# Kernel tuning notes

Measured on AMD Instinct MI355X. Metric: run time of the kernel, lower is better.

The kernel has to match this reference:

```python
import jax, jax.numpy as jnp
import numpy as np
from jax import lax

PS = 4  # patchsize

def conv2d(x, w, b, pad, dil=1):
    y = lax.conv_general_dilated(x, w, (1, 1), [(pad, pad), (pad, pad)],
                                 rhs_dilation=(dil, dil),
                                 dimension_numbers=('NCHW', 'OIHW', 'NCHW'))
    return y + b[None, :, None, None]

def instance_norm(x, eps=1e-5):
    mu = x.mean(axis=(2, 3), keepdims=True)
    var = x.var(axis=(2, 3), keepdims=True)
    return (x - mu) / jnp.sqrt(var + eps)

def lrelu(x):
    return jnp.where(x >= 0, x, 0.2 * x)

def setup_inputs() -> dict:
    key = jax.random.key(0)
    ks = jax.random.split(key, 20)
    B, C, H, W = 16, 256, 64, 64
    nh, nw = H // PS, W // PS
    N = nh * nw
    s = 0.05
    return {
        'x': jax.random.normal(ks[0], (B, C, H, W), jnp.float32),
        'mask': jax.random.uniform(ks[1], (B, 1, H, W), jnp.float32),
        'dis': jax.random.normal(ks[2], (N, N), jnp.float32),
        'lap_a': jnp.ones((1,), jnp.float32),
        'Wq': jax.random.normal(ks[3], (C, C, 1, 1), jnp.float32) * s,
        'bq': jax.random.normal(ks[4], (C,), jnp.float32) * s,
        'Wk': jax.random.normal(ks[5], (C, C, 1, 1), jnp.float32) * s,
        'bk': jax.random.normal(ks[6], (C,), jnp.float32) * s,
        'Wv': jax.random.normal(ks[7], (C, C, 1, 1), jnp.float32) * s,
        'bv': jax.random.normal(ks[8], (C,), jnp.float32) * s,
        'noise_q': jax.random.normal(ks[9], (B, C, nh, PS, nw, PS), jnp.float32),
        'noise_k': jax.random.normal(ks[10], (B, C, nh, PS, nw, PS), jnp.float32),
        'noise_v': jax.random.normal(ks[11], (B, C, nh, PS, nw, PS), jnp.float32),
        'W_out': jax.random.normal(ks[12], (C, C, 3, 3), jnp.float32) * s,
        'b_out': jax.random.normal(ks[13], (C,), jnp.float32) * s,
        'W1': jax.random.normal(ks[14], (C, C, 3, 3), jnp.float32) * s,
        'b1': jax.random.normal(ks[15], (C,), jnp.float32) * s,
        'W2': jax.random.normal(ks[16], (C, C, 3, 3), jnp.float32) * s,
        'b2': jax.random.normal(ks[17], (C,), jnp.float32) * s,
    }

def _patchify(t, noise, B, C, nh, nw):
    # (B,C,H,W) -> (B,C,nh,PS,nw,PS) + noise -> (B, nh*nw, C*PS*PS)
    t = t.reshape(B, C, nh, PS, nw, PS) + noise
    t = t.transpose(0, 2, 4, 1, 3, 5).reshape(B, nh * nw, C * PS * PS)
    return t

def reference(x, mask, dis, lap_a, Wq, bq, Wk, bk, Wv, bv,
              noise_q, noise_k, noise_v, W_out, b_out, W1, b1, W2, b2):
    B, C, H, W = x.shape
    nh, nw = H // PS, W // PS
    N = nh * nw
    head = PS * 4
    Cp = C * PS * PS
    d = Cp // head

    residual = x
    q = _patchify(conv2d(x, Wq, bq, 0), noise_q, B, C, nh, nw)
    k = _patchify(conv2d(x, Wk, bk, 0), noise_k, B, C, nh, nw)
    v = _patchify(conv2d(x, Wv, bv, 0), noise_v, B, C, nh, nw)

    dis_b = jax.nn.softplus(lap_a)[0] * dis  # (N, N)

    qh = q.reshape(B, N, head, d)
    kh = k.reshape(B, N, head, d)
    vh = v.reshape(B, N, head, d)

    # scores: (head, B, N, N); bias added BEFORE scaling, as in the original
    scores = jnp.einsum('bnhd,bmhd->hbnm', qh, kh)
    scores = (scores + dis_b) / jnp.sqrt(jnp.asarray(d, scores.dtype))

    # mask: patch mean < 0.5 masks key positions
    m = mask.reshape(B, 1, nh, PS, nw, PS).transpose(0, 2, 4, 1, 3, 5)
    m = m.reshape(B, N, PS * PS).mean(-1) < 0.5  # (B, N) bool
    m = jnp.broadcast_to(m[:, None, :], (B, N, N))  # (B, N, N)
    scores = jnp.where(m[None], -jnp.inf, scores)

    p = jax.nn.softmax(scores, axis=-1)
    out = jnp.einsum('hbnm,bmhd->bnhd', p, vh).reshape(B, N, Cp)

    # un-patchify: (B,N,Cp) -> (B,nh,nw,C,PS,PS) -> (B,C,H,W)
    out = out.reshape(B, nh, nw, C, PS, PS).transpose(0, 3, 1, 4, 2, 5).reshape(B, C, H, W)
    out = lrelu(conv2d(out, W_out, b_out, 1)) + residual

    # feed-forward: conv(dil=2) -> IN -> lrelu -> conv -> IN -> lrelu, residual
    y = lrelu(instance_norm(conv2d(out, W1, b1, 2, dil=2)))
    y = lrelu(instance_norm(conv2d(y, W2, b2, 1)))
    return out + y
```

## Files before the change

### kernel.cpp

```cpp
#include <hip/hip_runtime.h>
#include <cstdint>
#include <cstddef>

typedef _Float16 f16;
typedef _Float16 f16x8 __attribute__((ext_vector_type(8)));
typedef _Float16 f16x4 __attribute__((ext_vector_type(4)));
typedef float    f32x4 __attribute__((ext_vector_type(4)));

#define MFMA16(a,b,c) __builtin_amdgcn_mfma_f32_16x16x32_f16((a),(b),(c),0,0,0)

__device__ __forceinline__ float lrelu(float v){ return v >= 0.f ? v : 0.2f*v; }

__device__ __forceinline__ void async_copy16(const f16* g, f16* l){
  __builtin_amdgcn_global_load_lds(
      (const __attribute__((address_space(1))) void*)(uintptr_t)(const void*)g,
      (__attribute__((address_space(3))) void*)(uint32_t)(uintptr_t)(void*)l,
      16, 0, 0);
}


__global__ __launch_bounds__(256) void k_prep1x1(
    const float* __restrict__ wq, const float* __restrict__ wk, const float* __restrict__ wv,
    f16* __restrict__ oq, f16* __restrict__ ok, f16* __restrict__ ov)
{
  int i = blockIdx.x*256 + threadIdx.x;
  int sel = i >> 16, r = i & 65535;
  const float* s = sel==0 ? wq : (sel==1 ? wk : wv);
  f16* d = sel==0 ? oq : (sel==1 ? ok : ov);
  d[r] = (f16)s[r];
}

__global__ __launch_bounds__(256) void k_prep3x3(
    const float* __restrict__ w0, const float* __restrict__ w1, const float* __restrict__ w2,
    f16* __restrict__ o0, f16* __restrict__ o1, f16* __restrict__ o2)
{
  int i = blockIdx.x*256 + threadIdx.x;
  int sel = i / 589824;
  int r = i - sel*589824;
  int t = r >> 16; int rr = r & 65535; int co = rr >> 8; int ci = rr & 255;
  const float* s = sel==0 ? w0 : (sel==1 ? w1 : w2);
  f16* d = sel==0 ? o0 : (sel==1 ? o1 : o2);
  d[r] = (f16)s[(co*256 + ci)*9 + t];
}

__global__ __launch_bounds__(256) void k_pmask(const float* __restrict__ mask, float* __restrict__ pm)
{
  int t = blockIdx.x*256 + threadIdx.x;
  int b = t >> 8, n = t & 255;
  int y0 = (n>>4)<<2, x0 = (n&15)<<2;
  const float* mb = mask + b*4096;
  float s = 0.f;
  #pragma unroll
  for (int i=0;i<4;++i)
    #pragma unroll
    for (int j=0;j<4;++j) s += mb[(y0+i)*64 + x0+j];
  pm[t] = (s*(1.f/16.f) < 0.5f) ? 1.f : 0.f;
}

__global__ __launch_bounds__(256) void k_nchw2nhwc(
    const float* __restrict__ src, const float2* __restrict__ st, f16* __restrict__ dst)
{
  int idx = blockIdx.x;
  int y = idx & 63, b = idx >> 6;
  int tid = threadIdx.x;
  __shared__ f16 T[64*264];

  {
    const float* row = src + (size_t)(b*256+tid)*4096 + y*64;
    float mu = 0.f, ri = 1.f;
    bool doin = (st != nullptr);
    if (doin){ float2 s = st[b*256+tid]; mu = s.x; ri = s.y; }
    #pragma unroll
    for (int j=0;j<16;++j){
      float4 u = *(const float4*)(row + j*4);
      int x = j*4;
      float a0=(u.x-mu)*ri, a1=(u.y-mu)*ri, a2=(u.z-mu)*ri, a3=(u.w-mu)*ri;
      if (doin){ a0=lrelu(a0); a1=lrelu(a1); a2=lrelu(a2); a3=lrelu(a3); }
      T[(x+0)*264+tid]=(f16)a0; T[(x+1)*264+tid]=(f16)a1;
      T[(x+2)*264+tid]=(f16)a2; T[(x+3)*264+tid]=(f16)a3;
    }
  }
  __syncthreads();
  {
    int oct = tid & 31, pxl = tid >> 5;
    #pragma unroll
    for (int p=0;p<8;++p){
      int px = p*8 + pxl;
      *(uint4*)&dst[((size_t)((b*64+y)*64+px)<<8) + oct*8] = *(const uint4*)&T[px*264 + oct*8];
    }
  }
}

__global__ __launch_bounds__(256, 4) void k_qkv(
    const f16* __restrict__ xh,
    const f16* __restrict__ wq, const f16* __restrict__ wk, const f16* __restrict__ wv,
    const float* __restrict__ bq, const float* __restrict__ bk, const float* __restrict__ bv,
    const float* __restrict__ nq, const float* __restrict__ nk, const float* __restrict__ nv,
    f16* __restrict__ Qp, f16* __restrict__ Kp, f16* __restrict__ Vt)
{
  int idx = blockIdx.x;
  int yt  = idx & 15; idx >>= 4;
  int cot = idx & 3;  idx >>= 2;
  int b   = idx & 15; idx >>= 4;
  int sel = idx;
  int tid = threadIdx.x;
  int wave = tid>>6, lane = tid&63, quad = lane>>4, l16 = lane&15;
  int co0 = cot*64, y0 = yt*4;

  const f16*  W    = sel==0 ? wq : (sel==1 ? wk : wv);
  const float* bias= sel==0 ? bq : (sel==1 ? bk : bv);
  const float* nz  = sel==0 ? nq : (sel==1 ? nk : nv);

  __shared__ f16 smem[20480];

  f32x4 acc[16];
  #pragma unroll
  for (int i=0;i<16;++i){ acc[i][0]=0.f; acc[i][1]=0.f; acc[i][2]=0.f; acc[i][3]=0.f; }

  int g8 = (((lane&3) ^ ((lane>>3)&3)) << 3);
  const f16* Wrow = W + ((co0 + wave*16 + (lane>>2))<<8) + g8;
  const f16* Xrow = xh + (((size_t)((b*64 + y0)*64))<<8) + g8;

  auto stage = [&](int buf, int kc){
    int ci0 = kc<<5;
    f16* Ab = smem + buf*2048;
    f16* Bb = smem + 4096 + buf*8192;
    async_copy16(Wrow + ci0, Ab + wave*512);
    #pragma unroll
    for (int j=0;j<4;++j){
      int px = j*64 + wave*16 + (lane>>2);
      async_copy16(Xrow + ((size_t)px<<8) + ci0, Bb + (j*64 + wave*16)*32);
    }
  };

  stage(0, 0);
  #pragma unroll
  for (int kc=0; kc<8; ++kc){
    int cur = kc & 1;
    if (kc < 7){
      stage(cur^1, kc+1);
      asm volatile("s_waitcnt vmcnt(5)\n\ts_barrier" ::: "memory");
    } else {
      asm volatile("s_waitcnt vmcnt(0)\n\ts_barrier" ::: "memory");
    }
    const f16* Al = smem + cur*2048;
    const f16* Bl = smem + 4096 + cur*8192;
    f16x8 af = *(const f16x8*)&Al[(wave*16+l16)*32 + ((quad ^ ((l16>>1)&3))<<3)];
    #pragma unroll
    for (int nt=0;nt<16;++nt){
      int bidx = (nt>>2)*64 + (nt&3)*16 + l16;
      f16x8 bf = *(const f16x8*)&Bl[bidx*32 + ((quad ^ ((bidx>>1)&3))<<3)];
      acc[nt] = MFMA16(af, bf, acc[nt]);
    }
    asm volatile("s_waitcnt lgkmcnt(0)\n\ts_barrier" ::: "memory");
  }

  int cob = co0 + wave*16 + quad*4;
  int h0 = cot*4, pr = yt;
  float bs[4];
  #pragma unroll
  for (int r=0;r<4;++r) bs[r] = bias[cob+r];

  const float* nzb = nz + ((size_t)(b*256 + co0) << 12) + y0*64;

  #pragma unroll
  for (int half=0; half<2; ++half){
    #pragma unroll
    for (int p=0;p<8;++p){
      int i = p*256 + tid;
      int c32 = i>>6, px0 = (i&63)*4;
      float4 u = *(const float4*)(nzb + (((size_t)(half*32 + c32))<<12) + px0);
      f16x4 h4; h4[0]=(f16)u.x; h4[1]=(f16)u.y; h4[2]=(f16)u.z; h4[3]=(f16)u.w;
      *(f16x4*)&smem[c32*256 + (px0 ^ (((c32>>2)&3)<<4))] = h4;
    }
    __syncthreads();
    if ((wave>>1) == half){
      #pragma unroll
      for (int nt=0;nt<16;++nt){
        int px = (nt>>2)*64 + (nt&3)*16 + l16;
        int n_ = (nt&3)*4 + (l16>>2);
        int ddb = (quad<<6) + ((nt>>2)<<2) + (l16&3);
        #pragma unroll
        for (int r=0;r<4;++r){
          int c32 = ((wave&1)<<4) + (quad<<2) + r;
          float nzv = (float)smem[c32*256 + (px ^ (((c32>>2)&3)<<4))];
          float v = acc[nt][r] + bs[r] + nzv;
          int dd = ddb + (r<<4);
          if (sel < 2){
            int row = ((wave&1)<<4) + n_;
            smem[8192 + row*280 + dd + ((dd>>6)<<3)] = (f16)v;
          } else {
            smem[8192 + ((wave&1)*4128) + dd*16 + ((dd>>6)<<3) + n_] = (f16)v;
          }
        }
      }
    }
    __syncthreads();
    if (sel < 2){
      f16* dst = sel==0 ? Qp : Kp;
      #pragma unroll
      for (int pass=0; pass<4; ++pass){
        int rowi = pass*8 + (tid>>5);
        int ch  = tid & 31;
        uint4 v = *(const uint4*)&smem[8192 + rowi*280 + ch*8 + ((ch>>3)<<3)];
        int grow = half*32 + rowi;
        *(uint4*)&dst[((b*16 + h0 + (grow>>4))<<16) + ((pr*16 + (grow&15))<<8) + ch*8] = v;
      }
    } else {
      #pragma unroll
      for (int p=0;p<4;++p){
        int i = p*256 + tid;
        int rw = i>>1, hf = i&1;
        int dd = rw & 255;
        uint4 v = *(const uint4*)&smem[8192 + (rw>>8)*4128 + dd*16 + ((dd>>6)<<3) + hf*8];
        *(uint4*)&Vt[((b*16 + h0 + half*2 + (rw>>8))<<16) + (dd<<8) + pr*16 + hf*8] = v;
      }
    }
    __syncthreads();
  }
}

__global__ __launch_bounds__(256) void k_attn(
    const f16* __restrict__ Qp, const f16* __restrict__ Kp, const f16* __restrict__ Vt,
    const float* __restrict__ dis, const float* __restrict__ lap_a,
    const float* __restrict__ pm, f16* __restrict__ attn)
{
  int idx = blockIdx.x;
  int nt = idx & 3; idx >>= 2;
  int h  = idx & 15; idx >>= 4;
  int b  = idx;
  int tid = threadIdx.x, wave = tid>>6, lane = tid&63, quad = lane>>4, l16 = lane&15;
  int n0 = nt*64;
  int bh = (b*16 + h) << 16;

  __shared__ f16 smem[25344];
  f16* Ql  = smem;
  f16* KVl = smem + 16896;

  {
    int row = tid>>2, part = (tid&3)*64;
    const uint4* s = (const uint4*)&Qp[bh + ((n0+row)<<8) + part];
    uint4* d = (uint4*)&Ql[row*264 + part];
    #pragma unroll
    for (int j=0;j<8;++j) d[j] = s[j];
  }

  float splus = log1pf(expf(lap_a[0]));

  f32x4 sacc[16];
  #pragma unroll
  for (int i=0;i<16;++i){ sacc[i][0]=0.f; sacc[i][1]=0.f; sacc[i][2]=0.f; sacc[i][3]=0.f; }

  #pragma unroll
  for (int mc=0; mc<8; ++mc){
    __syncthreads();
    {
      int row = tid>>3, part = (tid&7)*32;
      const uint4* s = (const uint4*)&Kp[bh + ((mc*32+row)<<8) + part];
      uint4* d = (uint4*)&KVl[row*264 + part];
      #pragma unroll
      for (int j=0;j<4;++j) d[j] = s[j];
    }
    __syncthreads();
    #pragma unroll
    for (int kk=0;kk<8;++kk){
      f16x8 af = *(const f16x8*)&Ql[(wave*16+l16)*264 + kk*32 + quad*8];
      #pragma unroll
      for (int j=0;j<2;++j){
        f16x8 bf = *(const f16x8*)&KVl[(j*16+l16)*264 + kk*32 + quad*8];
        sacc[mc*2+j] = MFMA16(af, bf, sacc[mc*2+j]);
      }
    }
  }

  int nrow_base = wave*16 + quad*4;
  float pmv[16];
  #pragma unroll
  for (int t=0;t<16;++t) pmv[t] = pm[b*256 + t*16 + l16];

  #pragma unroll
  for (int r=0;r<4;++r){
    int n = n0 + nrow_base + r;
    float sv[16];
    float mx = -1e30f;
    #pragma unroll
    for (int t=0;t<16;++t){
      float s = sacc[t][r];
      s = (s + splus * dis[n*256 + t*16 + l16]) * 0.0625f;
      s = (pmv[t] > 0.5f) ? -1e30f : s;
      sv[t] = s;
      mx = fmaxf(mx, s);
    }
    #pragma unroll
    for (int off=1; off<16; off<<=1) mx = fmaxf(mx, __shfl_xor(mx, off, 64));
    float sum = 0.f;
    #pragma unroll
    for (int t=0;t<16;++t){ float e = __expf(sv[t]-mx); sv[t]=e; sum += e; }
    #pragma unroll
    for (int off=1; off<16; off<<=1) sum += __shfl_xor(sum, off, 64);
    float inv = 1.f/sum;
    #pragma unroll
    for (int t=0;t<16;++t) Ql[(nrow_base + r)*264 + t*16 + l16] = (f16)(sv[t]*inv);
  }

  f32x4 oacc[16];
  #pragma unroll
  for (int i=0;i<16;++i){ oacc[i][0]=0.f; oacc[i][1]=0.f; oacc[i][2]=0.f; oacc[i][3]=0.f; }

  for (int dc=0; dc<8; ++dc){
    __syncthreads();
    {
      int row = tid>>3, part = (tid&7)*32;
      const uint4* s = (const uint4*)&Vt[bh + ((dc*32+row)<<8) + part];
      uint4* d = (uint4*)&KVl[row*264 + part];
      #pragma unroll
      for (int j=0;j<4;++j) d[j] = s[j];
    }
    __syncthreads();
    #pragma unroll
    for (int kk=0;kk<8;++kk){
      f16x8 af = *(const f16x8*)&Ql[(wave*16+l16)*264 + kk*32 + quad*8];
      #pragma unroll
      for (int j=0;j<2;++j){
        f16x8 bf = *(const f16x8*)&KVl[(j*16+l16)*264 + kk*32 + quad*8];
        oacc[dc*2+j] = MFMA16(af, bf, oacc[dc*2+j]);
      }
    }
  }

  __syncthreads();
  #pragma unroll
  for (int dc=0; dc<8; ++dc){
    #pragma unroll
    for (int j=0;j<2;++j){
      int dd = dc*32 + j*16 + l16;
      int c_ = dd>>4;
      int pi = (dd>>2)&3, pj = dd&3;
      #pragma unroll
      for (int r=0;r<4;++r){
        int nl = nrow_base + r;
        int y_ = ((nl>>4)<<2) + pi;
        int x  = ((nl&15)<<2) + pj;
        smem[(y_*64 + x)*24 + c_] = (f16)oacc[dc*2+j][r];
      }
    }
  }
  __syncthreads();
  #pragma unroll
  for (int p=0;p<4;++p){
    int pix = p*256 + tid;
    int y_ = pix>>6, x = pix&63;
    uint4 v0 = *(const uint4*)&smem[pix*24];
    uint4 v1 = *(const uint4*)&smem[pix*24 + 8];
    size_t o = ((size_t)((b*64 + nt*16 + y_)*64 + x)<<8) + h*16;
    *(uint4*)&attn[o]     = v0;
    *(uint4*)&attn[o + 8] = v1;
  }
}

template<int DIL, int MODE>
__global__ __launch_bounds__(256) void k_conv3(
    const f16* __restrict__ in, const f16* __restrict__ Wt, const float* __restrict__ bias,
    const float* __restrict__ resid, float* __restrict__ outf, f16* __restrict__ outh)
{
  int idx = blockIdx.x;
  int yt  = idx & 15; idx >>= 4;
  int cot = idx & 3;  idx >>= 2;
  int b   = idx;
  int y0 = yt*4, co0 = cot*64;
  int tid = threadIdx.x;
  int wave = tid>>6, lane = tid&63, quad = lane>>4, l16 = lane&15;

  __shared__ float cs4[8192];
  f16* Al = (f16*)cs4;
  f16* Bl = (f16*)cs4 + 7680;

  f32x4 acc[16];
  #pragma unroll
  for (int i=0;i<16;++i){ acc[i][0]=0.f; acc[i][1]=0.f; acc[i][2]=0.f; acc[i][3]=0.f; }

  constexpr int PXR = 64 + 2*DIL;
  constexpr int NU4 = 16*PXR;

  for (int ky=0; ky<3; ++ky){
    int yb = y0 + DIL*(ky-1);
    for (int kc=0; kc<8; ++kc){
      int ci0 = kc*32;
      {
        int aco = tid>>2, ap = (tid&3)*8;
        #pragma unroll
        for (int kx=0;kx<3;++kx)
          *(uint4*)&Al[kx*2560 + aco*40 + ap] =
              *(const uint4*)&Wt[((ky*3+kx)<<16) + ((co0+aco)<<8) + ci0 + ap];
      }
      #pragma unroll
      for (int p=0;p<5;++p){
        int i = p*256 + tid;
        if (i < NU4){
          int px = i>>2, oct = i&3;
          int yr = px / PXR, xp = px - yr*PXR;
          int yy = yb + yr, xx = xp - DIL;
          uint4 v = make_uint4(0u,0u,0u,0u);
          if (yy>=0 && yy<64 && xx>=0 && xx<64)
            v = *(const uint4*)&in[((size_t)((b*64+yy)*64+xx)<<8) + ci0 + oct*8];
          int si = yr*68 + xp;
          *(uint4*)&Bl[si*32 + ((oct ^ ((si>>1)&3))<<3)] = v;
        }
      }
      __syncthreads();
      #pragma unroll
      for (int kx=0;kx<3;++kx){
        f16x8 af = *(const f16x8*)&Al[kx*2560 + (wave*16+l16)*40 + quad*8];
        #pragma unroll
        for (int nt=0;nt<16;++nt){
          int bidx = (nt>>2)*68 + (nt&3)*16 + l16 + kx*DIL;
          f16x8 bf = *(const f16x8*)&Bl[bidx*32 + ((quad ^ ((bidx>>1)&3))<<3)];
          acc[nt] = MFMA16(af, bf, acc[nt]);
        }
      }
      __syncthreads();
    }
  }

  int cob = co0 + wave*16 + quad*4;
  float bs[4];
  #pragma unroll
  for (int r=0;r<4;++r) bs[r] = bias[cob+r];

  if (MODE==0){
    const float* rb = resid + ((size_t)(b*256 + co0) << 12) + y0*64;
    #pragma unroll
    for (int half=0; half<2; ++half){
      #pragma unroll
      for (int p=0;p<8;++p){
        int i = p*256 + tid;
        int c32 = i>>6, px0 = (i&63)*4;
        float4 u = *(const float4*)(rb + (((size_t)(half*32 + c32))<<12) + px0);
        *(float4*)&cs4[c32*256 + (px0 ^ (((c32>>2)&3)<<3))] = u;
      }
      __syncthreads();
      if ((wave>>1) == half){
        #pragma unroll
        for (int nt=0;nt<16;++nt){
          int y = y0 + (nt>>2), x = (nt&3)*16 + l16;
          int px = (nt>>2)*64 + (nt&3)*16 + l16;
          #pragma unroll
          for (int r=0;r<4;++r){
            int co = cob + r;
            int c32 = ((wave&1)<<4) + (quad<<2) + r;
            float rv = cs4[c32*256 + (px ^ (((c32>>2)&3)<<3))];
            float v = lrelu(acc[nt][r] + bs[r]) + rv;
            size_t o = (size_t)(b*256+co)*4096 + y*64 + x;
            outf[o] = v;
            outh[((size_t)((b*64+y)*64+x)<<8) + co] = (f16)v;
          }
        }
      }
      __syncthreads();
    }
  } else {
    #pragma unroll
    for (int nt=0;nt<16;++nt){
      int y = y0 + (nt>>2), x = (nt&3)*16 + l16;
      #pragma unroll
      for (int r=0;r<4;++r){
        int co = cob + r;
        float v = acc[nt][r] + bs[r];
        size_t o = (size_t)(b*256+co)*4096 + y*64 + x;
        outf[o] = v;
      }
    }
  }
}

__global__ __launch_bounds__(256) void k_instats(const float* __restrict__ v, float2* __restrict__ st)
{
  int bc = blockIdx.x;
  const float* p = v + (size_t)bc*4096;
  int tid = threadIdx.x;
  float s=0.f, ss=0.f;
  #pragma unroll
  for (int it=0; it<4; ++it){
    float4 u = *(const float4*)(p + it*1024 + tid*4);
    s  += u.x+u.y+u.z+u.w;
    ss += u.x*u.x + u.y*u.y + u.z*u.z + u.w*u.w;
  }
  #pragma unroll
  for (int off=32; off; off>>=1){ s += __shfl_down(s, off, 64); ss += __shfl_down(ss, off, 64); }
  __shared__ float rs[4], rss[4];
  int wave = tid>>6, lane = tid&63;
  if (lane==0){ rs[wave]=s; rss[wave]=ss; }
  __syncthreads();
  if (tid==0){
    float S = rs[0]+rs[1]+rs[2]+rs[3], SS = rss[0]+rss[1]+rss[2]+rss[3];
    float mu = S*(1.f/4096.f);
    float var = SS*(1.f/4096.f) - mu*mu;
    st[bc] = make_float2(mu, rsqrtf(var + 1e-5f));
  }
}

__global__ __launch_bounds__(256) void k_final(float* __restrict__ out, const float* __restrict__ c2,
                                               const float2* __restrict__ st)
{
  int i4 = blockIdx.x*256 + threadIdx.x;
  float2 s = st[i4>>10];
  float4 u = *(const float4*)(c2 + (size_t)i4*4);
  float4 o = *(const float4*)(out + (size_t)i4*4);
  o.x += lrelu((u.x - s.x)*s.y);
  o.y += lrelu((u.y - s.x)*s.y);
  o.z += lrelu((u.z - s.x)*s.y);
  o.w += lrelu((u.w - s.x)*s.y);
  *(float4*)(out + (size_t)i4*4) = o;
}

extern "C" void kernel_launch(void* const* d_in, const int* in_sizes, int n_in,
                              void* d_out, int out_size, void* d_ws, size_t ws_size,
                              hipStream_t stream)
{
  const float* x    = (const float*)d_in[0];
  const float* mask = (const float*)d_in[1];
  const float* dis  = (const float*)d_in[2];
  const float* lapa = (const float*)d_in[3];
  const float* Wq   = (const float*)d_in[4];
  const float* bq   = (const float*)d_in[5];
  const float* Wk   = (const float*)d_in[6];
  const float* bk   = (const float*)d_in[7];
  const float* Wv   = (const float*)d_in[8];
  const float* bv   = (const float*)d_in[9];
  const float* nq   = (const float*)d_in[10];
  const float* nk   = (const float*)d_in[11];
  const float* nv   = (const float*)d_in[12];
  const float* Wo   = (const float*)d_in[13];
  const float* bo   = (const float*)d_in[14];
  const float* W1   = (const float*)d_in[15];
  const float* b1   = (const float*)d_in[16];
  const float* W2   = (const float*)d_in[17];
  const float* b2   = (const float*)d_in[18];

  char* w = (char*)d_ws;
  f16*   xh    = (f16*)(w + 0);
  f16*   Qp    = (f16*)(w + 33554432);
  f16*   Kp    = (f16*)(w + 67108864);
  f16*   Vt    = (f16*)(w + 100663296);
  f16*   attnb = (f16*)(w + 134217728);
  f16*   outbf = (f16*)(w + 0);
  float* c1    = (float*)(w + 33554432);
  f16*   y1    = (f16*)(w + 100663296);
  float* c2    = (float*)(w + 33554432);
  f16*   wqh   = (f16*)(w + 167772160);
  f16*   wkh   = wqh + 65536;
  f16*   wvh   = wkh + 65536;
  f16*   wt0   = (f16*)(w + 168165376);
  f16*   wt1   = wt0 + 589824;
  f16*   wt2   = wt1 + 589824;
  float* pmk   = (float*)(w + 171704320);
  float2* st1  = (float2*)(w + 171720704);
  float2* st2  = (float2*)(w + 171753472);
  float* out   = (float*)d_out;

  k_prep1x1<<<768, 256, 0, stream>>>(Wq, Wk, Wv, wqh, wkh, wvh);
  k_prep3x3<<<6912, 256, 0, stream>>>(Wo, W1, W2, wt0, wt1, wt2);
  k_pmask<<<16, 256, 0, stream>>>(mask, pmk);
  k_nchw2nhwc<<<1024, 256, 0, stream>>>(x, nullptr, xh);
  k_qkv<<<3072, 256, 0, stream>>>(xh, wqh, wkh, wvh, bq, bk, bv, nq, nk, nv, Qp, Kp, Vt);
  k_attn<<<1024, 256, 0, stream>>>(Qp, Kp, Vt, dis, lapa, pmk, attnb);
  k_conv3<1,0><<<1024, 256, 0, stream>>>(attnb, wt0, bo, x, out, outbf);
  k_conv3<2,1><<<1024, 256, 0, stream>>>(outbf, wt1, b1, nullptr, c1, nullptr);
  k_instats<<<4096, 256, 0, stream>>>(c1, st1);
  k_nchw2nhwc<<<1024, 256, 0, stream>>>(c1, st1, y1);
  k_conv3<1,1><<<1024, 256, 0, stream>>>(y1, wt2, b2, nullptr, c2, nullptr);
  k_instats<<<4096, 256, 0, stream>>>(c2, st2);
  k_final<<<16384, 256, 0, stream>>>(out, c2, st2);
}
```

Measured before the change: 963.5 us.

## Register-prefetch next conv3 tile and remap waves to rows for operand reuse

The 3x3 conv kernel now prefetches the next weight/input chunk into registers while the current chunk's MFMAs run, instead of doing a serial load-sync-compute loop. The wave-to-output mapping also changes: each wave owns one output row and all 64 output channels (a 4x4 MFMA tile grid). Each A and B fragment is then reused four times, so LDS reads per MFMA drop. The cost is more registers for the prefetch buffers and accumulators, which may lower occupancy, and an extra barrier per stage.

```diff
diff --git a/kernel.cpp b/kernel.cpp
--- a/kernel.cpp
+++ b/kernel.cpp
@@ -375,57 +375,97 @@
   f16* Al = (f16*)cs4;
   f16* Bl = (f16*)cs4 + 7680;
 
-  f32x4 acc[16];
-  #pragma unroll
-  for (int i=0;i<16;++i){ acc[i][0]=0.f; acc[i][1]=0.f; acc[i][2]=0.f; acc[i][3]=0.f; }
+  f32x4 acc[4][4];
+  #pragma unroll
+  for (int xi=0;xi<4;++xi)
+    #pragma unroll
+    for (int cq=0;cq<4;++cq){ acc[xi][cq][0]=0.f; acc[xi][cq][1]=0.f; acc[xi][cq][2]=0.f; acc[xi][cq][3]=0.f; }
 
   constexpr int PXR = 64 + 2*DIL;
   constexpr int NU4 = 16*PXR;
 
-  for (int ky=0; ky<3; ++ky){
+  int aco = tid>>2, ap = (tid&3)*8;
+
+  auto load_regs = [&](int t, uint4* rA, uint4* rB){
+    int ky = t>>3, kc = t&7, ci0 = kc*32;
     int yb = y0 + DIL*(ky-1);
-    for (int kc=0; kc<8; ++kc){
-      int ci0 = kc*32;
-      {
-        int aco = tid>>2, ap = (tid&3)*8;
+    #pragma unroll
+    for (int kx=0;kx<3;++kx)
+      rA[kx] = *(const uint4*)&Wt[((ky*3+kx)<<16) + ((co0+aco)<<8) + ci0 + ap];
+    #pragma unroll
+    for (int p=0;p<5;++p){
+      int i = p*256 + tid;
+      uint4 v = make_uint4(0u,0u,0u,0u);
+      if (i < NU4){
+        int px = i>>2, oct = i&3;
+        int yr = px / PXR, xp = px - yr*PXR;
+        int yy = yb + yr, xx = xp - DIL;
+        if (yy>=0 && yy<64 && xx>=0 && xx<64)
+          v = *(const uint4*)&in[((size_t)((b*64+yy)*64+xx)<<8) + ci0 + oct*8];
+      }
+      rB[p] = v;
+    }
+  };
+
+  auto store_lds = [&](const uint4* rA, const uint4* rB){
+    #pragma unroll
+    for (int kx=0;kx<3;++kx)
+      *(uint4*)&Al[kx*2560 + aco*40 + ap] = rA[kx];
+    #pragma unroll
+    for (int p=0;p<5;++p){
+      int i = p*256 + tid;
+      if (i < NU4){
+        int px = i>>2, oct = i&3;
+        int yr = px / PXR, xp = px - yr*PXR;
+        int si = yr*68 + xp;
+        *(uint4*)&Bl[si*32 + ((oct ^ ((si>>1)&3))<<3)] = rB[p];
+      }
+    }
+  };
+
+  auto mfma_phase = [&](){
+    #pragma unroll
+    for (int kx=0;kx<3;++kx){
+      f16x8 af[4], bfv[4];
+      #pragma unroll
+      for (int cq=0;cq<4;++cq)
+        af[cq] = *(const f16x8*)&Al[kx*2560 + (cq*16+l16)*40 + quad*8];
+      #pragma unroll
+      for (int xi=0;xi<4;++xi){
+        int bidx = wave*68 + xi*16 + l16 + kx*DIL;
+        bfv[xi] = *(const f16x8*)&Bl[bidx*32 + ((quad ^ ((bidx>>1)&3))<<3)];
+      }
+      #pragma unroll
+      for (int xi=0;xi<4;++xi)
         #pragma unroll
-        for (int kx=0;kx<3;++kx)
-          *(uint4*)&Al[kx*2560 + aco*40 + ap] =
-              *(const uint4*)&Wt[((ky*3+kx)<<16) + ((co0+aco)<<8) + ci0 + ap];
-      }
-      #pragma unroll
-      for (int p=0;p<5;++p){
-        int i = p*256 + tid;
-        if (i < NU4){
-          int px = i>>2, oct = i&3;
-          int yr = px / PXR, xp = px - yr*PXR;
-          int yy = yb + yr, xx = xp - DIL;
-          uint4 v = make_uint4(0u,0u,0u,0u);
-          if (yy>=0 && yy<64 && xx>=0 && xx<64)
-            v = *(const uint4*)&in[((size_t)((b*64+yy)*64+xx)<<8) + ci0 + oct*8];
-          int si = yr*68 + xp;
-          *(uint4*)&Bl[si*32 + ((oct ^ ((si>>1)&3))<<3)] = v;
-        }
-      }
-      __syncthreads();
-      #pragma unroll
-      for (int kx=0;kx<3;++kx){
-        f16x8 af = *(const f16x8*)&Al[kx*2560 + (wave*16+l16)*40 + quad*8];
-        #pragma unroll
-        for (int nt=0;nt<16;++nt){
-          int bidx = (nt>>2)*68 + (nt&3)*16 + l16 + kx*DIL;
-          f16x8 bf = *(const f16x8*)&Bl[bidx*32 + ((quad ^ ((bidx>>1)&3))<<3)];
-          acc[nt] = MFMA16(af, bf, acc[nt]);
-        }
-      }
-      __syncthreads();
-    }
-  }
-
-  int cob = co0 + wave*16 + quad*4;
-  float bs[4];
-  #pragma unroll
-  for (int r=0;r<4;++r) bs[r] = bias[cob+r];
+        for (int cq=0;cq<4;++cq)
+          acc[xi][cq] = MFMA16(af[cq], bfv[xi], acc[xi][cq]);
+    }
+  };
+
+  uint4 rA0[3], rB0[5], rA1[3], rB1[5];
+  load_regs(0, rA0, rB0);
+  for (int t=0; t<24; t+=2){
+    __syncthreads();
+    if (t+1 < 24) load_regs(t+1, rA1, rB1);
+    store_lds(rA0, rB0);
+    __syncthreads();
+    mfma_phase();
+
+    __syncthreads();
+    if (t+2 < 24) load_regs(t+2, rA0, rB0);
+    store_lds(rA1, rB1);
+    __syncthreads();
+    mfma_phase();
+  }
+  __syncthreads();
+
+  int y = y0 + wave;
+  float bsv[4][4];
+  #pragma unroll
+  for (int cq=0;cq<4;++cq)
+    #pragma unroll
+    for (int r=0;r<4;++r) bsv[cq][r] = bias[co0 + cq*16 + quad*4 + r];
 
   if (MODE==0){
     const float* rb = resid + ((size_t)(b*256 + co0) << 12) + y0*64;
@@ -439,17 +479,19 @@
         *(float4*)&cs4[c32*256 + (px0 ^ (((c32>>2)&3)<<3))] = u;
       }
       __syncthreads();
-      if ((wave>>1) == half){
+      #pragma unroll
+      for (int cq2=0; cq2<2; ++cq2){
+        int cq = half*2 + cq2;
         #pragma unroll
-        for (int nt=0;nt<16;++nt){
-          int y = y0 + (nt>>2), x = (nt&3)*16 + l16;
-          int px = (nt>>2)*64 + (nt&3)*16 + l16;
+        for (int xi=0; xi<4; ++xi){
+          int x = xi*16 + l16;
+          int px = wave*64 + xi*16 + l16;
           #pragma unroll
           for (int r=0;r<4;++r){
-            int co = cob + r;
-            int c32 = ((wave&1)<<4) + (quad<<2) + r;
+            int co = co0 + cq*16 + quad*4 + r;
+            int c32 = cq2*16 + quad*4 + r;
             float rv = cs4[c32*256 + (px ^ (((c32>>2)&3)<<3))];
-            float v = lrelu(acc[nt][r] + bs[r]) + rv;
+            float v = lrelu(acc[xi][cq][r] + bsv[cq][r]) + rv;
             size_t o = (size_t)(b*256+co)*4096 + y*64 + x;
             outf[o] = v;
             outh[((size_t)((b*64+y)*64+x)<<8) + co] = (f16)v;
@@ -460,14 +502,17 @@
     }
   } else {
     #pragma unroll
-    for (int nt=0;nt<16;++nt){
-      int y = y0 + (nt>>2), x = (nt&3)*16 + l16;
-      #pragma unroll
-      for (int r=0;r<4;++r){
-        int co = cob + r;
-        float v = acc[nt][r] + bs[r];
-        size_t o = (size_t)(b*256+co)*4096 + y*64 + x;
-        outf[o] = v;
+    for (int xi=0; xi<4; ++xi){
+      int x = xi*16 + l16;
+      #pragma unroll
+      for (int cq=0;cq<4;++cq){
+        #pragma unroll
+        for (int r=0;r<4;++r){
+          int co = co0 + cq*16 + quad*4 + r;
+          float v = acc[xi][cq][r] + bsv[cq][r];
+          size_t o = (size_t)(b*256+co)*4096 + y*64 + x;
+          outf[o] = v;
+        }
       }
     }
   }
```

Result: faster. 923.7 us (-4.1%).
